# Optimization experiments

Measured on AMD Instinct MI355X. Metric: run time of the kernel, lower is better.

The kernel has to match this reference:

```python
import jax, jax.numpy as jnp
import numpy as np
from jax import lax

DIM = 256
HEADS = 8
DIM_HEAD = 32
INNER = HEADS * DIM_HEAD  # 256
SCALE = DIM_HEAD ** -0.5
EPS = 1e-5
DN = ('NCHW', 'OIHW', 'NCHW')


def chan_layer_norm(x, g):
    # LayerNorm over channel dim (axis=1), biased variance
    mean = jnp.mean(x, axis=1, keepdims=True)
    var = jnp.mean((x - mean) ** 2, axis=1, keepdims=True)
    return (x - mean) / jnp.sqrt(var + EPS) * g


def conv1x1(x, w):
    return lax.conv_general_dilated(x, w, (1, 1), 'VALID', dimension_numbers=DN)


def dwconv3x3(x, w):
    # depthwise 3x3, padding=1, groups=channels; w: [C,1,3,3]
    return lax.conv_general_dilated(x, w, (1, 1), 'SAME', dimension_numbers=DN,
                                    feature_group_count=x.shape[1])


def setup_inputs() -> dict:
    key = jax.random.key(0)
    ks = jax.random.split(key, 9)
    B, X, Y = 16, 64, 64
    fmap = jax.random.normal(ks[0], (B, DIM, X, Y), dtype=jnp.float32)
    w = lambda k, shape: (jax.random.normal(k, shape, dtype=jnp.float32) * 0.02)
    return {
        'fmap': fmap,
        'g_norm': jnp.ones((1, DIM, 1, 1), dtype=jnp.float32),
        'wq1': w(ks[1], (INNER, DIM, 1, 1)),
        'wq_dw': w(ks[2], (INNER, 1, 3, 3)),
        'wk1': w(ks[3], (INNER, DIM, 1, 1)),
        'wk_dw': w(ks[4], (INNER, 1, 3, 3)),
        'wv1': w(ks[5], (INNER, DIM, 1, 1)),
        'wv_dw': w(ks[6], (INNER, 1, 3, 3)),
        'wo': w(ks[7], (DIM, INNER, 1, 1)),
        'g_out': jnp.ones((1, DIM, 1, 1), dtype=jnp.float32),
    }


def reference(fmap, g_norm, wq1, wq_dw, wk1, wk_dw, wv1, wv_dw, wo, g_out):
    b, _, X, Y = fmap.shape
    n = X * Y
    x = chan_layer_norm(fmap, g_norm)
    # QKV: 1x1 conv -> depthwise 3x3 conv (dropout is identity in eval)
    q = dwconv3x3(conv1x1(x, wq1), wq_dw)
    k = dwconv3x3(conv1x1(x, wk1), wk_dw)
    v = dwconv3x3(conv1x1(x, wv1), wv_dw)
    # b (h c) x y -> b h n c
    def split(t):
        return t.reshape(b, HEADS, DIM_HEAD, n).transpose(0, 1, 3, 2)
    q, k, v = split(q), split(k), split(v)
    q = jax.nn.softmax(q, axis=-1) * SCALE   # softmax over feature dim
    k = jax.nn.softmax(k, axis=-2)           # softmax over sequence dim
    ctx = jnp.einsum('bhnd,bhne->bhde', k, v)    # [b,h,d,d]
    out = jnp.einsum('bhnd,bhde->bhne', q, ctx)  # [b,h,n,d]
    # b h n d -> b (h d) x y
    out = out.transpose(0, 1, 3, 2).reshape(b, INNER, X, Y)
    out = jax.nn.silu(out)
    out = conv1x1(out, wo)
    return chan_layer_norm(out, g_out)
```

## Files before the change

### kernel.cpp

```cpp
#include <hip/hip_runtime.h>


typedef unsigned short u16;
typedef __bf16 bf16x8 __attribute__((ext_vector_type(8)));
typedef float f32x4 __attribute__((ext_vector_type(4)));
typedef float f32x16 __attribute__((ext_vector_type(16)));

#define DEV static __device__ __forceinline__

DEV float b2f(u16 u) { return __uint_as_float(((unsigned int)u) << 16); }
DEV u16 f2bf(float f) {
  unsigned int u = __float_as_uint(f);
  return (u16)((u + 0x7fffu + ((u >> 16) & 1u)) >> 16);
}
DEV void gl2lds16(const void* g, void* l) {
  __builtin_amdgcn_global_load_lds((__attribute__((address_space(1))) void*)g,
                                   (__attribute__((address_space(3))) void*)l, 16, 0, 0);
}

__global__ __launch_bounds__(256) void prep_kernel(const float* __restrict__ wk,
                                                   const float* __restrict__ wv,
                                                   const float* __restrict__ wq,
                                                   const float* __restrict__ wo,
                                                   u16* __restrict__ wb) {
  const int i = blockIdx.x * 256 + threadIdx.x;
  const float* src = (blockIdx.y == 0) ? wk : (blockIdx.y == 1) ? wv : (blockIdx.y == 2) ? wq : wo;
  wb[blockIdx.y * 65536 + i] = f2bf(src[i]);
}

__global__ __launch_bounds__(256) void ln_tin_kernel(const float* __restrict__ f,
                                                     const float* __restrict__ g,
                                                     u16* __restrict__ xT) {
  __shared__ u16 tile[64 * 258];
  __shared__ float red[2 * 256];
  __shared__ float mu_s[64], inv_s[64];
  const int t = threadIdx.x;
  const int p0 = blockIdx.x * 64;
  const int b = blockIdx.y;
  const long fb = (long)b * 256 * 4096;
  const int p = t & 63, cg = t >> 6;
  float s1 = 0.f, s2 = 0.f;
  for (int pass = 0; pass < 64; ++pass) {
    int c = pass * 4 + cg;
    float v = f[fb + (long)c * 4096 + p0 + p];
    s1 += v; s2 += v * v;
    tile[p * 258 + c] = f2bf(v);
  }
  red[cg * 64 + p] = s1;
  red[256 + cg * 64 + p] = s2;
  __syncthreads();
  if (t < 64) {
    float a1 = red[t] + red[64 + t] + red[128 + t] + red[192 + t];
    float a2 = red[256 + t] + red[320 + t] + red[384 + t] + red[448 + t];
    float mu = a1 * (1.f / 256.f);
    float var = a2 * (1.f / 256.f) - mu * mu;
    mu_s[t] = mu;
    inv_s[t] = 1.0f / sqrtf(var + 1e-5f);
  }
  __syncthreads();
  {
    float gc = g[t];
    for (int pp = 0; pp < 64; ++pp) {
      float v = b2f(tile[pp * 258 + t]);
      xT[((long)b * 4096 + p0 + pp) * 256 + t] = f2bf((v - mu_s[pp]) * inv_s[pp] * gc);
    }
  }
}

__global__ __launch_bounds__(256) void gemm_bt_kernel(
    const u16* __restrict__ A, const u16* __restrict__ B0, const u16* __restrict__ B1,
    u16* __restrict__ Cg, int ldc, long sA, long sC) {
  __shared__ u16 As[128 * 32];
  __shared__ u16 Bs[128 * 32];
  const int t = threadIdx.x;
  const int wave = t >> 6, lane = t & 63, quad = lane >> 4, l16 = lane & 15;
  const int wr = wave >> 1, wc = wave & 1;
  const int m0 = blockIdx.x * 128;
  const int jt = blockIdx.y;
  const int b = blockIdx.z;
  const u16* Ab = A + (long)b * sA + (long)m0 * 256;
  const u16* Bt = (jt < 2 ? B0 : B1) + (jt & 1) * 128 * 256;
  u16* Cb = Cg + (long)b * sC + (long)m0 * ldc + jt * 128;

  const int srow = lane >> 2;
  const int scol = (lane & 3) * 8;
  f32x4 acc[4][4];
#pragma unroll
  for (int i = 0; i < 4; ++i)
#pragma unroll
    for (int j = 0; j < 4; ++j) acc[i][j] = (f32x4){0.f, 0.f, 0.f, 0.f};

  const int aoff = (wr * 64 + l16) * 32 + quad * 8;
  const int boff = (wc * 64 + l16) * 32 + quad * 8;

  for (int ks = 0; ks < 8; ++ks) {
    const int k0 = ks * 32;
    __syncthreads();
    for (int i = wave; i < 8; i += 4) {
      gl2lds16(Ab + (i * 16 + srow) * 256 + k0 + scol, &As[i * 512 + lane * 8]);
      gl2lds16(Bt + (i * 16 + srow) * 256 + k0 + scol, &Bs[i * 512 + lane * 8]);
    }
    __syncthreads();
    bf16x8 af[4], bfr[4];
#pragma unroll
    for (int mt = 0; mt < 4; ++mt) af[mt] = *(const bf16x8*)&As[aoff + mt * 512];
#pragma unroll
    for (int nt = 0; nt < 4; ++nt) bfr[nt] = *(const bf16x8*)&Bs[boff + nt * 512];
#pragma unroll
    for (int mt = 0; mt < 4; ++mt)
#pragma unroll
      for (int nt = 0; nt < 4; ++nt)
        acc[mt][nt] = __builtin_amdgcn_mfma_f32_16x16x32_bf16(af[mt], bfr[nt], acc[mt][nt], 0, 0, 0);
  }
#pragma unroll
  for (int mt = 0; mt < 4; ++mt) {
    const int mbase = wr * 64 + mt * 16 + quad * 4;
#pragma unroll
    for (int nt = 0; nt < 4; ++nt) {
      const int n = wc * 64 + nt * 16 + l16;
#pragma unroll
      for (int r = 0; r < 4; ++r)
        Cb[(long)(mbase + r) * ldc + n] = f2bf(acc[mt][nt][r]);
    }
  }
}

__global__ __launch_bounds__(256) void dwq_kernel(const u16* __restrict__ qT,
                                                  const float* __restrict__ wdw,
                                                  u16* __restrict__ qp) {
  const int t = threadIdx.x;
  const int strip = blockIdx.x, h = blockIdx.y, b = blockIdx.z;
  const int x0 = strip * 4;
  const int wave = t >> 6, lane = t & 63;
  const int ysel = lane & 15, cg = lane >> 4;
  const int y = wave * 16 + ysel;
  float w[72];
#pragma unroll
  for (int q = 0; q < 8; ++q)
#pragma unroll
    for (int i = 0; i < 9; ++i) w[q * 9 + i] = wdw[(h * 32 + cg * 8 + q) * 9 + i];
  const u16* qb = qT + (long)b * 4096 * 256 + h * 32 + cg * 8;
  u16* ob = qp + ((long)b * 4096 + y) * 256 + h * 32 + cg * 8;

#pragma unroll
  for (int it = 0; it < 4; ++it) {
    const int x = x0 + it;
    float acc[8] = {0.f, 0.f, 0.f, 0.f, 0.f, 0.f, 0.f, 0.f};
#pragma unroll
    for (int r = 0; r < 3; ++r) {
      const int xx = x - 1 + r;
#pragma unroll
      for (int dy = 0; dy < 3; ++dy) {
        const int yy = y - 1 + dy;
        if (((unsigned)xx < 64u) & ((unsigned)yy < 64u)) {
          uint4 pk = *(const uint4*)(qb + (long)(xx * 64 + yy) * 256);
          const u16* s = (const u16*)&pk;
#pragma unroll
          for (int q = 0; q < 8; ++q)
            acc[q] = fmaf(w[q * 9 + r * 3 + dy], b2f(s[q]), acc[q]);
        }
      }
    }
    float e[8];
    float s = 0.f;
#pragma unroll
    for (int q = 0; q < 8; ++q) { e[q] = __expf(acc[q]); s += e[q]; }
    s += __shfl_xor(s, 16);
    s += __shfl_xor(s, 32);
    const float inv = 0.17677669529663687f / s;
    uint4 o;
    u16* os = (u16*)&o;
#pragma unroll
    for (int q = 0; q < 8; ++q) os[q] = f2bf(e[q] * inv);
    *(uint4*)(ob + (long)x * 16384) = o;
  }
}

__global__ __launch_bounds__(1024, 4) void ctx_kernel(const u16* __restrict__ kvT,
                                                      const float* __restrict__ wkdw,
                                                      const float* __restrict__ wvdw,
                                                      float* __restrict__ par0,
                                                      float* __restrict__ par1) {
  __shared__ float redb[8 * 1088];
  __shared__ float redk[16 * 32];
  const int t = threadIdx.x;
  const int strip = blockIdx.x, h = blockIdx.y, b = blockIdx.z;
  const int wave = t >> 6, lane = t & 63;
  const int g = wave >> 2, wq = wave & 3;
  const int x0 = strip * 32 + g * 8;
  const int c = lane & 31, half = lane >> 5;
  const int ystart = wq * 16 + half * 8;
  float wk[9], wv[9];
#pragma unroll
  for (int i = 0; i < 9; ++i) {
    wk[i] = wkdw[(h * 32 + c) * 9 + i];
    wv[i] = wvdw[(h * 32 + c) * 9 + i];
  }
  const u16* kb = kvT + (long)b * 4096 * 512 + h * 32 + c;

  float fk[3][10], fv[3][10];
#pragma unroll
  for (int r = 0; r < 2; ++r) {
    const int x = x0 - 1 + r;
#pragma unroll
    for (int m = 0; m < 10; ++m) {
      const int yy = ystart - 1 + m;
      float a = 0.f, bb = 0.f;
      if (((unsigned)x < 64u) & ((unsigned)yy < 64u)) {
        const u16* p = kb + (long)(x * 64 + yy) * 512;
        a = b2f(p[0]);
        bb = b2f(p[256]);
      }
      fk[r][m] = a; fv[r][m] = bb;
    }
  }
  f32x16 acc;
#pragma unroll
  for (int r = 0; r < 16; ++r) acc[r] = 0.f;
  float ks = 0.f;

  for (int it = 0; it < 8; ++it) {
    const int x = x0 + it;
    {
      const int xn = x + 1;
#pragma unroll
      for (int m = 0; m < 10; ++m) {
        const int yy = ystart - 1 + m;
        float a = 0.f, bb = 0.f;
        if (((unsigned)xn < 64u) & ((unsigned)yy < 64u)) {
          const u16* p = kb + (long)(xn * 64 + yy) * 512;
          a = b2f(p[0]);
          bb = b2f(p[256]);
        }
        fk[2][m] = a; fv[2][m] = bb;
      }
    }
    union { bf16x8 v; u16 s[8]; } af, bf_;
#pragma unroll
    for (int j = 0; j < 8; ++j) {
      float a = 0.f, bb = 0.f;
#pragma unroll
      for (int r = 0; r < 3; ++r)
#pragma unroll
        for (int dy = 0; dy < 3; ++dy) {
          a = fmaf(wk[r * 3 + dy], fk[r][j + dy], a);
          bb = fmaf(wv[r * 3 + dy], fv[r][j + dy], bb);
        }
      const u16 eb = f2bf(__expf(a));
      ks += b2f(eb);
      af.s[j] = eb;
      bf_.s[j] = f2bf(bb);
    }
    acc = __builtin_amdgcn_mfma_f32_32x32x16_bf16(af.v, bf_.v, acc, 0, 0, 0);
#pragma unroll
    for (int m = 0; m < 10; ++m) {
      fk[0][m] = fk[1][m]; fk[1][m] = fk[2][m];
      fv[0][m] = fv[1][m]; fv[1][m] = fv[2][m];
    }
  }
  ks += __shfl_xor(ks, 32);
  if (half == 0) redk[wave * 32 + c] = ks;
  if (wave >= 8) {
#pragma unroll
    for (int r = 0; r < 16; ++r) redb[(wave - 8) * 1088 + lane * 17 + r] = acc[r];
  }
  __syncthreads();
  if (wave < 8) {
#pragma unroll
    for (int r = 0; r < 16; ++r) acc[r] += redb[wave * 1088 + lane * 17 + r];
  }
  __syncthreads();
  if (wave >= 4 && wave < 8) {
#pragma unroll
    for (int r = 0; r < 16; ++r) redb[(wave - 4) * 1088 + lane * 17 + r] = acc[r];
  }
  __syncthreads();
  if (wave < 4) {
#pragma unroll
    for (int r = 0; r < 16; ++r) acc[r] += redb[wave * 1088 + lane * 17 + r];
  }
  __syncthreads();
  if (wave >= 1 && wave < 4) {
#pragma unroll
    for (int r = 0; r < 16; ++r) redb[(wave - 1) * 1088 + lane * 17 + r] = acc[r];
  }
  __syncthreads();
  if (wave == 0) {
    float* par = (strip ? par1 : par0) + (long)(b * 8 + h) * 1056;
#pragma unroll
    for (int r = 0; r < 16; ++r) {
      float sum = acc[r] + redb[lane * 17 + r] + redb[1088 + lane * 17 + r] +
                  redb[2176 + lane * 17 + r];
      const int d = (r & 3) + 8 * (r >> 2) + 4 * half;
      par[d * 32 + c] = sum;
    }
    if (t < 32) {
      float s = 0.f;
#pragma unroll
      for (int w = 0; w < 16; ++w) s += redk[w * 32 + t];
      par[1024 + t] = s;
    }
  }
}

__global__ __launch_bounds__(256) void reduce_kernel(const float* __restrict__ par0,
                                                     const float* __restrict__ par1,
                                                     float* __restrict__ ctxF,
                                                     float* __restrict__ ksF) {
  const int bh = blockIdx.x;
  const long base = (long)bh * 1056;
  for (int i = threadIdx.x; i < 1056; i += 256) {
    float v = par0[base + i] + par1[base + i];
    if (i < 1024) ctxF[(long)bh * 1024 + i] = v;
    else ksF[(long)bh * 32 + (i - 1024)] = v;
  }
}

__global__ __launch_bounds__(256) void attn_kernel(const u16* __restrict__ qp,
                                                   const float* __restrict__ ctxg,
                                                   const float* __restrict__ ksumg,
                                                   u16* __restrict__ sout) {
  __shared__ float ctxn[8192];
  __shared__ u16 qlds[64 * 40];
  const int t = threadIdx.x;
  const int p0 = blockIdx.x * 64;
  const int b = blockIdx.y;
  for (int i = 0; i < 32; ++i) {
    int idx = i * 256 + t;
    ctxn[idx] = ctxg[(long)b * 8192 + idx] / ksumg[(long)b * 256 + (idx >> 5)];
  }
  __syncthreads();
  const int e = t & 31, pg = t >> 5;
  const int lr = t >> 2, lc = t & 3;
  float cc[32];
  for (int h = 0; h < 8; ++h) {
    __syncthreads();
    *(uint4*)&qlds[lr * 40 + lc * 8] =
        *(const uint4*)&qp[((long)b * 4096 + p0 + lr) * 256 + h * 32 + lc * 8];
#pragma unroll
    for (int d = 0; d < 32; ++d) cc[d] = ctxn[(h * 32 + d) * 32 + e];
    __syncthreads();
    for (int k = 0; k < 8; ++k) {
      int p = pg + k * 8;
      float a = 0.f;
#pragma unroll
      for (int jq = 0; jq < 4; ++jq) {
        bf16x8 qv = *(const bf16x8*)&qlds[p * 40 + jq * 8];
#pragma unroll
        for (int jj = 0; jj < 8; ++jj) a = fmaf((float)qv[jj], cc[jq * 8 + jj], a);
      }
      float sl = a / (1.f + __expf(-a));
      sout[((long)b * 4096 + p0 + p) * 256 + h * 32 + e] = f2bf(sl);
    }
  }
}

__global__ __launch_bounds__(256) void ln_tout_kernel(const u16* __restrict__ y,
                                                      const float* __restrict__ gout,
                                                      float* __restrict__ out) {
  __shared__ u16 tile[64 * 258];
  __shared__ float red[2 * 256];
  __shared__ float mu_s[64], inv_s[64];
  const int t = threadIdx.x;
  const int p0 = blockIdx.x * 64;
  const int b = blockIdx.y;
  for (int p = 0; p < 64; ++p)
    tile[p * 258 + t] = y[((long)b * 4096 + p0 + p) * 256 + t];
  __syncthreads();
  {
    const int p = t & 63, part = t >> 6;
    float s1 = 0.f, s2 = 0.f;
    for (int k = 0; k < 64; ++k) {
      float v = b2f(tile[p * 258 + part * 64 + k]);
      s1 += v; s2 += v * v;
    }
    red[part * 64 + p] = s1;
    red[256 + part * 64 + p] = s2;
  }
  __syncthreads();
  if (t < 64) {
    float s1 = red[t] + red[64 + t] + red[128 + t] + red[192 + t];
    float s2 = red[256 + t] + red[320 + t] + red[384 + t] + red[448 + t];
    float mu = s1 * (1.f / 256.f);
    float var = s2 * (1.f / 256.f) - mu * mu;
    mu_s[t] = mu;
    inv_s[t] = 1.0f / sqrtf(var + 1e-5f);
  }
  __syncthreads();
  {
    const int p = t & 63, cg = t >> 6;
    const long ob = (long)b * 256 * 4096;
    for (int pass = 0; pass < 64; ++pass) {
      int c = pass * 4 + cg;
      float v = b2f(tile[p * 258 + c]);
      out[ob + (long)c * 4096 + p0 + p] = (v - mu_s[p]) * inv_s[p] * gout[c];
    }
  }
}

extern "C" void kernel_launch(void* const* d_in, const int* in_sizes, int n_in,
                              void* d_out, int out_size, void* d_ws, size_t ws_size,
                              hipStream_t stream) {
  (void)in_sizes; (void)n_in; (void)out_size; (void)ws_size;
  const float* fmap = (const float*)d_in[0];
  const float* gnorm = (const float*)d_in[1];
  const float* wq1 = (const float*)d_in[2];
  const float* wqdw = (const float*)d_in[3];
  const float* wk1 = (const float*)d_in[4];
  const float* wkdw = (const float*)d_in[5];
  const float* wv1 = (const float*)d_in[6];
  const float* wvdw = (const float*)d_in[7];
  const float* wo = (const float*)d_in[8];
  const float* gout = (const float*)d_in[9];
  float* out = (float*)d_out;
  char* ws = (char*)d_ws;

  float* par0 = (float*)(ws);
  u16* wb = (u16*)(ws + 540672);
  float* par1 = (float*)(ws + 1064960);
  u16* wk_bf = wb;
  u16* wv_bf = wb + 65536;
  u16* wq_bf = wb + 131072;
  u16* wo_bf = wb + 196608;
  u16* xT = (u16*)(ws + 2097152);
  u16* kvT = (u16*)(ws + 35651584);
  u16* qT = kvT;
  float* ctxF = (float*)(ws + 35651584);
  float* ksF = (float*)(ws + 35651584 + 524288);
  u16* qp = (u16*)(ws + 69206016);
  u16* sbuf = xT;
  u16* ybuf = qp;

  prep_kernel<<<dim3(256, 4), 256, 0, stream>>>(wk1, wv1, wq1, wo, wb);
  ln_tin_kernel<<<dim3(64, 16), 256, 0, stream>>>(fmap, gnorm, xT);
  gemm_bt_kernel<<<dim3(32, 4, 16), 256, 0, stream>>>(xT, wk_bf, wv_bf, kvT, 512,
                                                      4096L * 256, 4096L * 512);
  ctx_kernel<<<dim3(2, 8, 16), 1024, 0, stream>>>(kvT, wkdw, wvdw, par0, par1);
  gemm_bt_kernel<<<dim3(32, 2, 16), 256, 0, stream>>>(xT, wq_bf, wq_bf, qT, 256,
                                                      4096L * 256, 4096L * 256);
  dwq_kernel<<<dim3(16, 8, 16), 256, 0, stream>>>(qT, wqdw, qp);
  reduce_kernel<<<dim3(128), 256, 0, stream>>>(par0, par1, ctxF, ksF);
  attn_kernel<<<dim3(64, 16), 256, 0, stream>>>(qp, ctxF, ksF, sbuf);
  gemm_bt_kernel<<<dim3(32, 2, 16), 256, 0, stream>>>(sbuf, wo_bf, wo_bf, ybuf, 256,
                                                      4096L * 256, 4096L * 256);
  ln_tout_kernel<<<dim3(64, 16), 256, 0, stream>>>(ybuf, gout, out);
}
```

Measured before the change: 347.7 us.

## Compute attention q·ctx with bf16 MFMA using hi/lo split context

Replaces the scalar FMA inner product in the attention kernel with MFMA 16x16x32 bf16 instructions. Each wave reads its q fragments directly from global memory. The normalized context matrix is stored in LDS as a bf16 hi/lo pair so that precision stays close to fp32. Each block now covers 128 positions instead of 64, halving the grid. The cost is two MFMAs per tile, and the output stores are scattered 2-byte writes.

```diff
diff --git a/kernel.cpp b/kernel.cpp
--- a/kernel.cpp
+++ b/kernel.cpp
@@ -320,37 +320,48 @@
                                                    const float* __restrict__ ctxg,
                                                    const float* __restrict__ ksumg,
                                                    u16* __restrict__ sout) {
-  __shared__ float ctxn[8192];
-  __shared__ u16 qlds[64 * 40];
-  const int t = threadIdx.x;
-  const int p0 = blockIdx.x * 64;
+  __shared__ u16 cnhi[8 * 32 * 40];
+  __shared__ u16 cnlo[8 * 32 * 40];
+  const int t = threadIdx.x;
+  const int p0 = blockIdx.x * 128;
   const int b = blockIdx.y;
-  for (int i = 0; i < 32; ++i) {
-    int idx = i * 256 + t;
-    ctxn[idx] = ctxg[(long)b * 8192 + idx] / ksumg[(long)b * 256 + (idx >> 5)];
-  }
-  __syncthreads();
-  const int e = t & 31, pg = t >> 5;
-  const int lr = t >> 2, lc = t & 3;
-  float cc[32];
+  const int wave = t >> 6, lane = t & 63, quad = lane >> 4, l16 = lane & 15;
+
+  for (int j = 0; j < 32; ++j) {
+    const int idx = j * 256 + t;
+    const int e = idx & 31, d = (idx >> 5) & 31, h = idx >> 10;
+    const float c = ctxg[(long)b * 8192 + idx] / ksumg[(long)b * 256 + (idx >> 5)];
+    const u16 hi = f2bf(c);
+    cnhi[h * 1280 + e * 40 + d] = hi;
+    cnlo[h * 1280 + e * 40 + d] = f2bf(c - b2f(hi));
+  }
+  __syncthreads();
+
+  const u16* qb = qp + ((long)b * 4096 + p0 + wave * 32) * 256;
+  u16* ob = sout + ((long)b * 4096 + p0 + wave * 32) * 256;
+#pragma unroll
   for (int h = 0; h < 8; ++h) {
-    __syncthreads();
-    *(uint4*)&qlds[lr * 40 + lc * 8] =
-        *(const uint4*)&qp[((long)b * 4096 + p0 + lr) * 256 + h * 32 + lc * 8];
-#pragma unroll
-    for (int d = 0; d < 32; ++d) cc[d] = ctxn[(h * 32 + d) * 32 + e];
-    __syncthreads();
-    for (int k = 0; k < 8; ++k) {
-      int p = pg + k * 8;
-      float a = 0.f;
-#pragma unroll
-      for (int jq = 0; jq < 4; ++jq) {
-        bf16x8 qv = *(const bf16x8*)&qlds[p * 40 + jq * 8];
-#pragma unroll
-        for (int jj = 0; jj < 8; ++jj) a = fmaf((float)qv[jj], cc[jq * 8 + jj], a);
+    const int cb = h * 1280 + quad * 8;
+    const bf16x8 bhi0 = *(const bf16x8*)&cnhi[cb + l16 * 40];
+    const bf16x8 bhi1 = *(const bf16x8*)&cnhi[cb + (16 + l16) * 40];
+    const bf16x8 blo0 = *(const bf16x8*)&cnlo[cb + l16 * 40];
+    const bf16x8 blo1 = *(const bf16x8*)&cnlo[cb + (16 + l16) * 40];
+#pragma unroll
+    for (int rt = 0; rt < 2; ++rt) {
+      const bf16x8 af = *(const bf16x8*)&qb[(rt * 16 + l16) * 256 + h * 32 + quad * 8];
+      f32x4 a0 = (f32x4){0.f, 0.f, 0.f, 0.f};
+      f32x4 a1 = (f32x4){0.f, 0.f, 0.f, 0.f};
+      a0 = __builtin_amdgcn_mfma_f32_16x16x32_bf16(af, blo0, a0, 0, 0, 0);
+      a0 = __builtin_amdgcn_mfma_f32_16x16x32_bf16(af, bhi0, a0, 0, 0, 0);
+      a1 = __builtin_amdgcn_mfma_f32_16x16x32_bf16(af, blo1, a1, 0, 0, 0);
+      a1 = __builtin_amdgcn_mfma_f32_16x16x32_bf16(af, bhi1, a1, 0, 0, 0);
+#pragma unroll
+      for (int r = 0; r < 4; ++r) {
+        const int row = rt * 16 + quad * 4 + r;
+        const float v0 = a0[r], v1 = a1[r];
+        ob[(long)row * 256 + h * 32 + l16] = f2bf(v0 / (1.f + __expf(-v0)));
+        ob[(long)row * 256 + h * 32 + 16 + l16] = f2bf(v1 / (1.f + __expf(-v1)));
       }
-      float sl = a / (1.f + __expf(-a));
-      sout[((long)b * 4096 + p0 + p) * 256 + h * 32 + e] = f2bf(sl);
     }
   }
 }
@@ -440,7 +451,7 @@
                                                       4096L * 256, 4096L * 256);
   dwq_kernel<<<dim3(16, 8, 16), 256, 0, stream>>>(qT, wqdw, qp);
   reduce_kernel<<<dim3(128), 256, 0, stream>>>(par0, par1, ctxF, ksF);
-  attn_kernel<<<dim3(64, 16), 256, 0, stream>>>(qp, ctxF, ksF, sbuf);
+  attn_kernel<<<dim3(32, 16), 256, 0, stream>>>(qp, ctxF, ksF, sbuf);
   gemm_bt_kernel<<<dim3(32, 2, 16), 256, 0, stream>>>(sbuf, wo_bf, wo_bf, ybuf, 256,
                                                       4096L * 256, 4096L * 256);
   ln_tout_kernel<<<dim3(64, 16), 256, 0, stream>>>(ybuf, gout, out);
```

Result: faster. 327.9 us (-5.7%).
